# Optimization experiments

Hardware: AMD Instinct MI355X
Metric: run time of the kernel (lower is better)

Reference implementation:

```python
import jax, jax.numpy as jnp
import numpy as np

HIDDEN = 1024
NUM_HEADS = 16
HEAD_DIM = HIDDEN // NUM_HEADS


def setup_inputs() -> dict:
    key = jax.random.key(0)
    k1, k2, k3 = jax.random.split(key, 3)
    x = jax.random.normal(k1, (2, 2048, HIDDEN), dtype=jnp.float32)
    # Linear weights, torch layout [out_features, in_features]
    w_qkv = jax.random.normal(k2, (3 * HIDDEN, HIDDEN), dtype=jnp.float32) * 0.02
    w_out = jax.random.normal(k3, (HIDDEN, HIDDEN), dtype=jnp.float32) * 0.02
    return {"x": x, "w_qkv": w_qkv, "w_out": w_out}


def reference(x, w_qkv, w_out):
    B, S, H = x.shape
    scale = 1.0 / HEAD_DIM ** 0.5
    qkv = jnp.einsum('bsh,oh->bso', x, w_qkv)              # [B,S,3H]
    qkv = qkv.reshape(B, S, 3, NUM_HEADS, HEAD_DIM)
    qkv = jnp.transpose(qkv, (2, 0, 3, 1, 4))               # [3,B,nh,S,hd]
    q, k, v = qkv[0], qkv[1], qkv[2]
    scores = jnp.einsum('bnsd,bntd->bnst', q, k) * scale    # [B,nh,S,S]
    attn = jax.nn.softmax(scores, axis=-1)
    out = jnp.einsum('bnst,bntd->bnsd', attn, v)            # [B,nh,S,hd]
    out = jnp.transpose(out, (0, 2, 1, 3)).reshape(B, S, H)
    return jnp.einsum('bsh,oh->bso', out, w_out)
```

## Files before the change

### kernel.cpp

```cpp
#include <hip/hip_runtime.h>
#include <stdint.h>

typedef unsigned short u16;
typedef __bf16 bf16x8 __attribute__((ext_vector_type(8)));
typedef float f32x4 __attribute__((ext_vector_type(4)));
typedef float f32x16 __attribute__((ext_vector_type(16)));
typedef unsigned u32x4 __attribute__((ext_vector_type(4)));

#define DEVI __device__ __forceinline__

typedef __attribute__((address_space(1))) void gvoid;
typedef __attribute__((address_space(3))) void lvoid;

DEVI u16 f2b(float f) {
  unsigned x = __builtin_bit_cast(unsigned, f);
  return (u16)((x + 0x7fffu + ((x >> 16) & 1u)) >> 16);
}

DEVI float exp2g(float x) { return __builtin_amdgcn_exp2f(x); }

DEVI void gload_lds16(const void* g, void* l) {
  __builtin_amdgcn_global_load_lds((gvoid*)g, (lvoid*)l, 16, 0, 0);
}

#define QSCALE 0.18033688011112042f

__global__ void cast_all(const float* __restrict__ x, const float* __restrict__ wqkv,
                         const float* __restrict__ wout, u16* __restrict__ outb) {
  int i = blockIdx.x * 256 + threadIdx.x;
  int stride = gridDim.x * 256;
  for (; i < 2097152; i += stride) {
    const float* src;
    float sc = 1.0f;
    if (i < 1048576) {
      src = x + 4 * (long)i;
    } else if (i < 1835008) {
      int j = i - 1048576;
      src = wqkv + 4 * (long)j;
      if (j < 262144) sc = QSCALE;
    } else {
      src = wout + 4 * (long)(i - 1835008);
    }
    float4 v = *(const float4*)src;
    ushort4 o;
    o.x = f2b(v.x * sc); o.y = f2b(v.y * sc); o.z = f2b(v.z * sc); o.w = f2b(v.w * sc);
    ((ushort4*)outb)[i] = o;
  }
}

template<int OUT, int TM>
__global__ __launch_bounds__(256)
void gemm_bt(const u16* __restrict__ A, const u16* __restrict__ B, void* __restrict__ Cv,
             void* __restrict__ Cv2, int M, int N, int K) {
  constexpr int MI = TM / 32;
  __shared__ u16 lA[TM * 64];
  __shared__ u16 lB[128 * 64];
  const int tid = threadIdx.x;
  const int lane = tid & 63;
  const int lr = lane & 15;
  const int lg = lane >> 4;
  const int wid = tid >> 6;
  const long bm = (long)blockIdx.y * TM;
  const long bn = (long)blockIdx.x * 128;
  const int wr = (wid >> 1) * (TM / 2);
  const int wc = (wid & 1) * 64;

  f32x4 acc[MI][4];
#pragma unroll
  for (int i = 0; i < MI; ++i)
#pragma unroll
    for (int j = 0; j < 4; ++j)
      acc[i][j] = (f32x4){0.f, 0.f, 0.f, 0.f};

  for (int k0 = 0; k0 < K; k0 += 64) {
#pragma unroll
    for (int q = 0; q < MI; ++q) {
      int bi = tid + q * 256;
      int row = bi >> 3;
      int col = ((bi & 7) ^ (row & 7)) * 8;
      gload_lds16(A + (bm + row) * (long)K + k0 + col, (char*)lA + bi * 16);
    }
#pragma unroll
    for (int q = 0; q < 4; ++q) {
      int bi = tid + q * 256;
      int row = bi >> 3;
      int col = ((bi & 7) ^ (row & 7)) * 8;
      gload_lds16(B + (bn + row) * (long)K + k0 + col, (char*)lB + bi * 16);
    }
    __syncthreads();
#pragma unroll
    for (int kk = 0; kk < 2; ++kk) {
      bf16x8 af[MI], bfr[4];
      int kb = kk * 4 + lg;
#pragma unroll
      for (int mi = 0; mi < MI; ++mi) {
        int row = wr + mi * 16 + lr;
        af[mi] = *(const bf16x8*)((const char*)lA + row * 128 + ((kb ^ (row & 7)) << 4));
      }
#pragma unroll
      for (int ni = 0; ni < 4; ++ni) {
        int row = wc + ni * 16 + lr;
        bfr[ni] = *(const bf16x8*)((const char*)lB + row * 128 + ((kb ^ (row & 7)) << 4));
      }
#pragma unroll
      for (int mi = 0; mi < MI; ++mi)
#pragma unroll
        for (int ni = 0; ni < 4; ++ni)
          acc[mi][ni] = __builtin_amdgcn_mfma_f32_16x16x32_bf16(af[mi], bfr[ni], acc[mi][ni], 0, 0, 0);
    }
    __syncthreads();
  }

  if (OUT == 2 && bn >= 2048) {
#pragma unroll
    for (int mi = 0; mi < MI; ++mi)
#pragma unroll
      for (int ni = 0; ni < 4; ++ni) {
        long tok = bm + wr + mi * 16 + lg * 4;
        long f = bn + wc + ni * 16 + lr - 2048;
        ushort4 st;
        st.x = f2b(acc[mi][ni][0]);
        st.y = f2b(acc[mi][ni][1]);
        st.z = f2b(acc[mi][ni][2]);
        st.w = f2b(acc[mi][ni][3]);
        u16* dst = (u16*)Cv2 + (((tok >> 11) << 4) + (f >> 6)) * 131072 + (f & 63) * 2048 + (tok & 2047);
        *(ushort4*)dst = st;
      }
  } else {
    const long strideN = (OUT == 2) ? 2048 : N;
#pragma unroll
    for (int mi = 0; mi < MI; ++mi)
#pragma unroll
      for (int ni = 0; ni < 4; ++ni)
#pragma unroll
        for (int r = 0; r < 4; ++r) {
          long row = bm + wr + mi * 16 + lg * 4 + r;
          long col = bn + wc + ni * 16 + lr;
          float v = acc[mi][ni][r];
          if (OUT == 1) ((float*)Cv)[row * strideN + col] = v;
          else          ((u16*)Cv)[row * strideN + col] = f2b(v);
        }
  }
}

__global__ __launch_bounds__(256, 2)
void attn_fwd(const u16* __restrict__ qk, const u16* __restrict__ vT,
              u16* __restrict__ outb) {
  __shared__ char SM[33280];

  const int tid = threadIdx.x;
  const int lane = tid & 63;
  const int wid = tid >> 6;
  const int ql = lane & 31;
  const int h  = lane >> 5;
  const int th = wid >> 1;
  const int qw = wid & 1;

  const int flat = blockIdx.x + (blockIdx.y << 4) + (blockIdx.z << 8);
  const int swz  = ((flat & 7) << 6) + (flat >> 3);
  const int qt = swz & 15;
  const int hd = (swz >> 4) & 15;
  const int b  = swz >> 8;

  const long rowbase = (long)b * 2048;
  const int qcol = hd * 64;
  const int kcol = 1024 + hd * 64;
  const int TSK = 64 * 2048;
  const long vhb = ((long)b * 16 + hd) * 131072;

  const int q0w = qt * 128 + qw * 64;
  bf16x8 qfA[4], qfB[4];
  {
    const u16* qpA = qk + (rowbase + q0w + ql) * 2048 + qcol + h * 8;
    const u16* qpB = qpA + 32 * 2048;
#pragma unroll
    for (int dblk = 0; dblk < 4; ++dblk) {
      qfA[dblk] = *(const bf16x8*)(qpA + dblk * 16);
      qfB[dblk] = *(const bf16x8*)(qpB + dblk * 16);
    }
  }

  float lA = 0.f, lB = 0.f;
  f32x16 oA[2], oB[2];
#pragma unroll
  for (int d = 0; d < 2; ++d)
#pragma unroll
    for (int r = 0; r < 16; ++r) { oA[d][r] = 0.f; oB[d][r] = 0.f; }

  const int c0 = tid, c1 = tid + 256;
  const int rk0 = c0 >> 3, ck0 = ((c0 & 7) ^ (rk0 & 7)) * 8;
  const int rk1 = c1 >> 3, ck1 = ((c1 & 7) ^ (rk1 & 7)) * 8;
  const int d0 = c0 * 16, d1 = c1 * 16;
  const u16* kp0 = qk + (rowbase + rk0) * 2048 + kcol + ck0;
  const u16* kp1 = qk + (rowbase + rk1) * 2048 + kcol + ck1;
  const u16* vp0 = vT + vhb + rk0 * 2048 + ck0;
  const u16* vp1 = vT + vhb + rk1 * 2048 + ck1;

  gload_lds16(kp0, SM + d0);          gload_lds16(kp1, SM + d1);
  gload_lds16(vp0, SM + 16384 + d0);  gload_lds16(vp1, SM + 16384 + d1);
  kp0 += TSK; kp1 += TSK; vp0 += 64; vp1 += 64;
  asm volatile("s_waitcnt vmcnt(0)" ::: "memory");
  __builtin_amdgcn_s_barrier();
  __builtin_amdgcn_sched_barrier(0);

  for (int tt = 0; tt < 16; ++tt) {
#pragma unroll
    for (int P = 0; P < 2; ++P) {
      char* KsCur = SM + P * 8192;
      char* VsCur = SM + 16384 + P * 8192;
      char* KsNxt = SM + (P ^ 1) * 8192;
      char* VsNxt = SM + 16384 + (P ^ 1) * 8192;

      gload_lds16(kp0, KsNxt + d0);  gload_lds16(kp1, KsNxt + d1);
      gload_lds16(vp0, VsNxt + d0);  gload_lds16(vp1, VsNxt + d1);
      kp0 += TSK; kp1 += TSK; vp0 += 64; vp1 += 64;

      f32x16 sA, sB;
#pragma unroll
      for (int r = 0; r < 16; ++r) { sA[r] = 0.f; sB[r] = 0.f; }
      const char* Kb = KsCur + (th * 32 + ql) * 128;
      __builtin_amdgcn_s_setprio(1);
#pragma unroll
      for (int kd = 0; kd < 4; ++kd) {
        bf16x8 kf = *(const bf16x8*)(Kb + (((kd * 2 + h) ^ (ql & 7)) << 4));
        sA = __builtin_amdgcn_mfma_f32_32x32x16_bf16(kf, qfA[kd], sA, 0, 0, 0);
        sB = __builtin_amdgcn_mfma_f32_32x32x16_bf16(kf, qfB[kd], sB, 0, 0, 0);
      }
      __builtin_amdgcn_s_setprio(0);

#pragma unroll
      for (int r = 0; r < 16; ++r) sA[r] = exp2g(sA[r]);
#pragma unroll
      for (int r = 0; r < 16; ++r) sB[r] = exp2g(sB[r]);
      lA += (((sA[0] + sA[1]) + (sA[2] + sA[3])) + ((sA[4] + sA[5]) + (sA[6] + sA[7])))
          + (((sA[8] + sA[9]) + (sA[10] + sA[11])) + ((sA[12] + sA[13]) + (sA[14] + sA[15])));
      lB += (((sB[0] + sB[1]) + (sB[2] + sB[3])) + ((sB[4] + sB[5]) + (sB[6] + sB[7])))
          + (((sB[8] + sB[9]) + (sB[10] + sB[11])) + ((sB[12] + sB[13]) + (sB[14] + sB[15])));

      unsigned wA[8], wB[8];
#pragma unroll
      for (int m = 0; m < 8; ++m) {
        asm("v_cvt_pk_bf16_f32 %0, %1, %2" : "=v"(wA[m]) : "v"(sA[2 * m]), "v"(sA[2 * m + 1]));
        asm("v_cvt_pk_bf16_f32 %0, %1, %2" : "=v"(wB[m]) : "v"(sB[2 * m]), "v"(sB[2 * m + 1]));
      }

      bf16x8 pbA[2], pbB[2];
#pragma unroll
      for (int ks = 0; ks < 2; ++ks) {
        unsigned a0 = wA[4 * ks],     a2 = wA[4 * ks + 2];
        unsigned a1 = wA[4 * ks + 1], a3 = wA[4 * ks + 3];
        asm("s_nop 1\n\tv_permlane32_swap_b32 %0, %1" : "+v"(a0), "+v"(a2));
        asm("s_nop 1\n\tv_permlane32_swap_b32 %0, %1" : "+v"(a1), "+v"(a3));
        u32x4 t; t[0] = a0; t[1] = a1; t[2] = a2; t[3] = a3;
        pbA[ks] = __builtin_bit_cast(bf16x8, t);
        unsigned b0 = wB[4 * ks],     b2 = wB[4 * ks + 2];
        unsigned b1 = wB[4 * ks + 1], b3 = wB[4 * ks + 3];
        asm("s_nop 1\n\tv_permlane32_swap_b32 %0, %1" : "+v"(b0), "+v"(b2));
        asm("s_nop 1\n\tv_permlane32_swap_b32 %0, %1" : "+v"(b1), "+v"(b3));
        u32x4 u; u[0] = b0; u[1] = b1; u[2] = b2; u[3] = b3;
        pbB[ks] = __builtin_bit_cast(bf16x8, u);
      }

      __builtin_amdgcn_s_setprio(1);
#pragma unroll
      for (int dblk = 0; dblk < 2; ++dblk) {
        const char* Vb = VsCur + (dblk * 32 + ql) * 128;
#pragma unroll
        for (int ks = 0; ks < 2; ++ks) {
          bf16x8 vf = *(const bf16x8*)(Vb + (((th * 4 + ks * 2 + h) ^ (ql & 7)) << 4));
          oA[dblk] = __builtin_amdgcn_mfma_f32_32x32x16_bf16(vf, pbA[ks], oA[dblk], 0, 0, 0);
          oB[dblk] = __builtin_amdgcn_mfma_f32_32x32x16_bf16(vf, pbB[ks], oB[dblk], 0, 0, 0);
        }
      }
      __builtin_amdgcn_s_setprio(0);

      asm volatile("s_waitcnt vmcnt(0)" ::: "memory");
      __builtin_amdgcn_s_barrier();
      __builtin_amdgcn_sched_barrier(0);
    }
  }
  __syncthreads();

  float pxA = lA, pyA = lA;
  asm("s_nop 1\n\tv_permlane32_swap_b32 %0, %1" : "+v"(pxA), "+v"(pyA));
  float lwA = lA + (h ? pxA : pyA);
  float pxB = lB, pyB = lB;
  asm("s_nop 1\n\tv_permlane32_swap_b32 %0, %1" : "+v"(pxB), "+v"(pyB));
  float lwB = lB + (h ? pxB : pyB);

  if (th == 1) {
    char* regA = SM + (qw * 2 + 0) * 8192;
    char* regB = SM + (qw * 2 + 1) * 8192;
#pragma unroll
    for (int dblk = 0; dblk < 2; ++dblk)
#pragma unroll
      for (int r = 0; r < 16; ++r) {
        int dl = dblk * 32 + (r & 3) + 8 * (r >> 2) + 4 * h;
        *(float*)(regA + dl * 128 + ql * 4) = oA[dblk][r];
        *(float*)(regB + dl * 128 + ql * 4) = oB[dblk][r];
      }
    if (h == 0) {
      *(float*)(SM + 32768 + (qw * 2 + 0) * 128 + ql * 4) = lwA;
      *(float*)(SM + 32768 + (qw * 2 + 1) * 128 + ql * 4) = lwB;
    }
  }
  __syncthreads();
  if (th == 0) {
    const char* regA = SM + (qw * 2 + 0) * 8192;
    const char* regB = SM + (qw * 2 + 1) * 8192;
#pragma unroll
    for (int dblk = 0; dblk < 2; ++dblk)
#pragma unroll
      for (int r = 0; r < 16; ++r) {
        int dl = dblk * 32 + (r & 3) + 8 * (r >> 2) + 4 * h;
        oA[dblk][r] += *(const float*)(regA + dl * 128 + ql * 4);
        oB[dblk][r] += *(const float*)(regB + dl * 128 + ql * 4);
      }
    float invA = 1.0f / (lwA + *(const float*)(SM + 32768 + (qw * 2 + 0) * 128 + ql * 4));
    float invB = 1.0f / (lwB + *(const float*)(SM + 32768 + (qw * 2 + 1) * 128 + ql * 4));
    long rowA = rowbase + q0w + ql;
    long rowB = rowA + 32;
#pragma unroll
    for (int dblk = 0; dblk < 2; ++dblk)
#pragma unroll
      for (int m = 0; m < 4; ++m) {
        ushort4 stA;
        stA.x = f2b(oA[dblk][4 * m + 0] * invA);
        stA.y = f2b(oA[dblk][4 * m + 1] * invA);
        stA.z = f2b(oA[dblk][4 * m + 2] * invA);
        stA.w = f2b(oA[dblk][4 * m + 3] * invA);
        *(ushort4*)(outb + rowA * 1024 + qcol + dblk * 32 + 8 * m + 4 * h) = stA;
        ushort4 stB;
        stB.x = f2b(oB[dblk][4 * m + 0] * invB);
        stB.y = f2b(oB[dblk][4 * m + 1] * invB);
        stB.z = f2b(oB[dblk][4 * m + 2] * invB);
        stB.w = f2b(oB[dblk][4 * m + 3] * invB);
        *(ushort4*)(outb + rowB * 1024 + qcol + dblk * 32 + 8 * m + 4 * h) = stB;
      }
  }
}

extern "C" void kernel_launch(void* const* d_in, const int* in_sizes, int n_in,
                              void* d_out, int out_size, void* d_ws, size_t ws_size,
                              hipStream_t stream) {
  const float* x     = (const float*)d_in[0];
  const float* w_qkv = (const float*)d_in[1];
  const float* w_out = (const float*)d_in[2];
  float* out = (float*)d_out;

  char* ws = (char*)d_ws;
  u16* xb    = (u16*)(ws);
  u16* wqkvb = (u16*)(ws + 8388608);
  u16* woutb = (u16*)(ws + 14680064);
  u16* qk    = (u16*)(ws + 16777216);
  u16* vT    = (u16*)(ws + 33554432);
  u16* attn  = (u16*)(ws + 41943040);

  cast_all<<<2048, 256, 0, stream>>>(x, w_qkv, w_out, xb);

  gemm_bt<2, 128><<<dim3(24, 32), 256, 0, stream>>>(xb, wqkvb, qk, vT, 4096, 3072, 1024);

  attn_fwd<<<dim3(16, 16, 2), 256, 0, stream>>>(qk, vT, attn);

  gemm_bt<1, 64><<<dim3(8, 64), 256, 0, stream>>>(attn, woutb, out, nullptr, 4096, 1024, 1024);
}
```

Before: 103.0 us.

## Double-buffer GEMM LDS tiles, remap blocks across XCDs, raise MFMA priority

The GEMM kernel now double-buffers its LDS tiles, so the global-to-LDS loads for the next K step are issued before the MFMAs on the current tile and memory latency overlaps compute. It also remaps block indices so consecutive tiles spread across the eight XCD chiplets, aiming for better L2 locality, and raises wave priority around the MFMA section. In exchange LDS use doubles, which may cut occupancy, and the remap assumes the block count divides evenly by eight.

```diff
diff --git a/kernel.cpp b/kernel.cpp
--- a/kernel.cpp
+++ b/kernel.cpp
@@ -53,15 +53,23 @@
 void gemm_bt(const u16* __restrict__ A, const u16* __restrict__ B, void* __restrict__ Cv,
              void* __restrict__ Cv2, int M, int N, int K) {
   constexpr int MI = TM / 32;
-  __shared__ u16 lA[TM * 64];
-  __shared__ u16 lB[128 * 64];
+  constexpr int ASZ = TM * 64;
+  __shared__ u16 lA[2 * ASZ];
+  __shared__ u16 lB[2 * 128 * 64];
   const int tid = threadIdx.x;
   const int lane = tid & 63;
   const int lr = lane & 15;
   const int lg = lane >> 4;
   const int wid = tid >> 6;
-  const long bm = (long)blockIdx.y * TM;
-  const long bn = (long)blockIdx.x * 128;
+
+  const int f = blockIdx.x + gridDim.x * blockIdx.y;
+  const int chunk = (gridDim.x * gridDim.y) >> 3;
+  const int ln = (f & 7) * chunk + (f >> 3);
+  const int bx = ln / gridDim.y;
+  const int by = ln % gridDim.y;
+  const long bm = (long)by * TM;
+  const long bn = (long)bx * 128;
+
   const int wr = (wid >> 1) * (TM / 2);
   const int wc = (wid & 1) * 64;
 
@@ -72,22 +80,37 @@
     for (int j = 0; j < 4; ++j)
       acc[i][j] = (f32x4){0.f, 0.f, 0.f, 0.f};
 
-  for (int k0 = 0; k0 < K; k0 += 64) {
+  auto stageA = [&](int buf, int k0) {
 #pragma unroll
     for (int q = 0; q < MI; ++q) {
       int bi = tid + q * 256;
       int row = bi >> 3;
       int col = ((bi & 7) ^ (row & 7)) * 8;
-      gload_lds16(A + (bm + row) * (long)K + k0 + col, (char*)lA + bi * 16);
-    }
+      gload_lds16(A + (bm + row) * (long)K + k0 + col, (char*)(lA + buf * ASZ) + bi * 16);
+    }
+  };
+  auto stageB = [&](int buf, int k0) {
 #pragma unroll
     for (int q = 0; q < 4; ++q) {
       int bi = tid + q * 256;
       int row = bi >> 3;
       int col = ((bi & 7) ^ (row & 7)) * 8;
-      gload_lds16(B + (bn + row) * (long)K + k0 + col, (char*)lB + bi * 16);
-    }
-    __syncthreads();
+      gload_lds16(B + (bn + row) * (long)K + k0 + col, (char*)(lB + buf * 128 * 64) + bi * 16);
+    }
+  };
+
+  stageA(0, 0); stageB(0, 0);
+  asm volatile("s_waitcnt vmcnt(0)" ::: "memory");
+  __builtin_amdgcn_s_barrier();
+  __builtin_amdgcn_sched_barrier(0);
+
+  const int NITER = K >> 6;
+  for (int it = 0; it < NITER; ++it) {
+    const int cur = it & 1;
+    if (it + 1 < NITER) { stageA(cur ^ 1, (it + 1) * 64); stageB(cur ^ 1, (it + 1) * 64); }
+
+    const u16* cA = lA + cur * ASZ;
+    const u16* cB = lB + cur * 128 * 64;
 #pragma unroll
     for (int kk = 0; kk < 2; ++kk) {
       bf16x8 af[MI], bfr[4];
@@ -95,20 +118,27 @@
 #pragma unroll
       for (int mi = 0; mi < MI; ++mi) {
         int row = wr + mi * 16 + lr;
-        af[mi] = *(const bf16x8*)((const char*)lA + row * 128 + ((kb ^ (row & 7)) << 4));
+        af[mi] = *(const bf16x8*)((const char*)cA + row * 128 + ((kb ^ (row & 7)) << 4));
       }
 #pragma unroll
       for (int ni = 0; ni < 4; ++ni) {
         int row = wc + ni * 16 + lr;
-        bfr[ni] = *(const bf16x8*)((const char*)lB + row * 128 + ((kb ^ (row & 7)) << 4));
-      }
+        bfr[ni] = *(const bf16x8*)((const char*)cB + row * 128 + ((kb ^ (row & 7)) << 4));
+      }
+      __builtin_amdgcn_s_setprio(1);
 #pragma unroll
       for (int mi = 0; mi < MI; ++mi)
 #pragma unroll
         for (int ni = 0; ni < 4; ++ni)
           acc[mi][ni] = __builtin_amdgcn_mfma_f32_16x16x32_bf16(af[mi], bfr[ni], acc[mi][ni], 0, 0, 0);
-    }
-    __syncthreads();
+      __builtin_amdgcn_s_setprio(0);
+    }
+
+    if (it + 1 < NITER) {
+      asm volatile("s_waitcnt vmcnt(0)" ::: "memory");
+      __builtin_amdgcn_s_barrier();
+      __builtin_amdgcn_sched_barrier(0);
+    }
   }
 
   if (OUT == 2 && bn >= 2048) {
@@ -117,13 +147,13 @@
 #pragma unroll
       for (int ni = 0; ni < 4; ++ni) {
         long tok = bm + wr + mi * 16 + lg * 4;
-        long f = bn + wc + ni * 16 + lr - 2048;
+        long ff = bn + wc + ni * 16 + lr - 2048;
         ushort4 st;
         st.x = f2b(acc[mi][ni][0]);
         st.y = f2b(acc[mi][ni][1]);
         st.z = f2b(acc[mi][ni][2]);
         st.w = f2b(acc[mi][ni][3]);
-        u16* dst = (u16*)Cv2 + (((tok >> 11) << 4) + (f >> 6)) * 131072 + (f & 63) * 2048 + (tok & 2047);
+        u16* dst = (u16*)Cv2 + (((tok >> 11) << 4) + (ff >> 6)) * 131072 + (ff & 63) * 2048 + (tok & 2047);
         *(ushort4*)dst = st;
       }
   } else {
```

After: 114.3 us. 10.9% more time.

## Split attention over two KV halves and add a combine kernel

Applied to the files above, without the earlier changes.

The attention kernel now splits the key/value sequence into two halves, so the grid doubles to 1024 blocks. Each block writes unnormalized bf16 partial outputs plus per-row softmax denominators to workspace buffers. A new elementwise kernel sums the two partials and normalizes them before the output projection GEMM. The aim is better CU occupancy during attention, at the cost of an extra launch, extra global traffic for the partials, and bf16 rounding of the unnormalized partials. The combine step does no max rescaling, so it is only correct if both halves use the same softmax offset.

```diff
diff --git a/kernel.cpp b/kernel.cpp
--- a/kernel.cpp
+++ b/kernel.cpp
@@ -16,6 +16,8 @@
   unsigned x = __builtin_bit_cast(unsigned, f);
   return (u16)((x + 0x7fffu + ((x >> 16) & 1u)) >> 16);
 }
+
+DEVI float b2f(u16 u) { return __builtin_bit_cast(float, (unsigned)u << 16); }
 
 DEVI float exp2g(float x) { return __builtin_amdgcn_exp2f(x); }
 
@@ -117,13 +119,13 @@
 #pragma unroll
       for (int ni = 0; ni < 4; ++ni) {
         long tok = bm + wr + mi * 16 + lg * 4;
-        long f = bn + wc + ni * 16 + lr - 2048;
+        long ff = bn + wc + ni * 16 + lr - 2048;
         ushort4 st;
         st.x = f2b(acc[mi][ni][0]);
         st.y = f2b(acc[mi][ni][1]);
         st.z = f2b(acc[mi][ni][2]);
         st.w = f2b(acc[mi][ni][3]);
-        u16* dst = (u16*)Cv2 + (((tok >> 11) << 4) + (f >> 6)) * 131072 + (f & 63) * 2048 + (tok & 2047);
+        u16* dst = (u16*)Cv2 + (((tok >> 11) << 4) + (ff >> 6)) * 131072 + (ff & 63) * 2048 + (tok & 2047);
         *(ushort4*)dst = st;
       }
   } else {
@@ -145,7 +147,7 @@
 
 __global__ __launch_bounds__(256, 2)
 void attn_fwd(const u16* __restrict__ qk, const u16* __restrict__ vT,
-              u16* __restrict__ outb) {
+              u16* __restrict__ po0, u16* __restrict__ po1, float* __restrict__ pl) {
   __shared__ char SM[33280];
 
   const int tid = threadIdx.x;
@@ -157,10 +159,12 @@
   const int qw = wid & 1;
 
   const int flat = blockIdx.x + (blockIdx.y << 4) + (blockIdx.z << 8);
-  const int swz  = ((flat & 7) << 6) + (flat >> 3);
+  const int swz  = ((flat & 7) << 7) + (flat >> 3);
   const int qt = swz & 15;
   const int hd = (swz >> 4) & 15;
-  const int b  = swz >> 8;
+  const int zz = swz >> 8;
+  const int b  = zz >> 1;
+  const int ts = zz & 1;
 
   const long rowbase = (long)b * 2048;
   const int qcol = hd * 64;
@@ -191,10 +195,10 @@
   const int rk0 = c0 >> 3, ck0 = ((c0 & 7) ^ (rk0 & 7)) * 8;
   const int rk1 = c1 >> 3, ck1 = ((c1 & 7) ^ (rk1 & 7)) * 8;
   const int d0 = c0 * 16, d1 = c1 * 16;
-  const u16* kp0 = qk + (rowbase + rk0) * 2048 + kcol + ck0;
-  const u16* kp1 = qk + (rowbase + rk1) * 2048 + kcol + ck1;
-  const u16* vp0 = vT + vhb + rk0 * 2048 + ck0;
-  const u16* vp1 = vT + vhb + rk1 * 2048 + ck1;
+  const u16* kp0 = qk + (rowbase + ts * 1024 + rk0) * 2048 + kcol + ck0;
+  const u16* kp1 = qk + (rowbase + ts * 1024 + rk1) * 2048 + kcol + ck1;
+  const u16* vp0 = vT + vhb + rk0 * 2048 + ts * 1024 + ck0;
+  const u16* vp1 = vT + vhb + rk1 * 2048 + ts * 1024 + ck1;
 
   gload_lds16(kp0, SM + d0);          gload_lds16(kp1, SM + d1);
   gload_lds16(vp0, SM + 16384 + d0);  gload_lds16(vp1, SM + 16384 + d1);
@@ -203,7 +207,7 @@
   __builtin_amdgcn_s_barrier();
   __builtin_amdgcn_sched_barrier(0);
 
-  for (int tt = 0; tt < 16; ++tt) {
+  for (int tt = 0; tt < 8; ++tt) {
 #pragma unroll
     for (int P = 0; P < 2; ++P) {
       char* KsCur = SM + P * 8192;
@@ -316,28 +320,64 @@
         oA[dblk][r] += *(const float*)(regA + dl * 128 + ql * 4);
         oB[dblk][r] += *(const float*)(regB + dl * 128 + ql * 4);
       }
-    float invA = 1.0f / (lwA + *(const float*)(SM + 32768 + (qw * 2 + 0) * 128 + ql * 4));
-    float invB = 1.0f / (lwB + *(const float*)(SM + 32768 + (qw * 2 + 1) * 128 + ql * 4));
+    float ltotA = lwA + *(const float*)(SM + 32768 + (qw * 2 + 0) * 128 + ql * 4);
+    float ltotB = lwB + *(const float*)(SM + 32768 + (qw * 2 + 1) * 128 + ql * 4);
+    if (h == 0) {
+      float* plb = pl + (long)ts * 65536 + ((long)b * 16 + hd) * 2048;
+      plb[q0w + ql]      = ltotA;
+      plb[q0w + 32 + ql] = ltotB;
+    }
     long rowA = rowbase + q0w + ql;
     long rowB = rowA + 32;
+    u16* pob = ts ? po1 : po0;
 #pragma unroll
     for (int dblk = 0; dblk < 2; ++dblk)
 #pragma unroll
       for (int m = 0; m < 4; ++m) {
         ushort4 stA;
-        stA.x = f2b(oA[dblk][4 * m + 0] * invA);
-        stA.y = f2b(oA[dblk][4 * m + 1] * invA);
-        stA.z = f2b(oA[dblk][4 * m + 2] * invA);
-        stA.w = f2b(oA[dblk][4 * m + 3] * invA);
-        *(ushort4*)(outb + rowA * 1024 + qcol + dblk * 32 + 8 * m + 4 * h) = stA;
+        stA.x = f2b(oA[dblk][4 * m + 0]);
+        stA.y = f2b(oA[dblk][4 * m + 1]);
+        stA.z = f2b(oA[dblk][4 * m + 2]);
+        stA.w = f2b(oA[dblk][4 * m + 3]);
+        *(ushort4*)(pob + rowA * 1024 + qcol + dblk * 32 + 8 * m + 4 * h) = stA;
         ushort4 stB;
-        stB.x = f2b(oB[dblk][4 * m + 0] * invB);
-        stB.y = f2b(oB[dblk][4 * m + 1] * invB);
-        stB.z = f2b(oB[dblk][4 * m + 2] * invB);
-        stB.w = f2b(oB[dblk][4 * m + 3] * invB);
-        *(ushort4*)(outb + rowB * 1024 + qcol + dblk * 32 + 8 * m + 4 * h) = stB;
-      }
-  }
+        stB.x = f2b(oB[dblk][4 * m + 0]);
+        stB.y = f2b(oB[dblk][4 * m + 1]);
+        stB.z = f2b(oB[dblk][4 * m + 2]);
+        stB.w = f2b(oB[dblk][4 * m + 3]);
+        *(ushort4*)(pob + rowB * 1024 + qcol + dblk * 32 + 8 * m + 4 * h) = stB;
+      }
+  }
+}
+
+__global__ __launch_bounds__(256)
+void attn_combine(u16* __restrict__ po0, const u16* __restrict__ po1,
+                  const float* __restrict__ pl) {
+  long i = (long)blockIdx.x * 256 + threadIdx.x;
+  long base = i * 8;
+  int row = (int)(base >> 10);
+  int col = (int)(base & 1023);
+  int hd = col >> 6;
+  int b = row >> 11;
+  int q = row & 2047;
+  long lidx = ((long)b * 16 + hd) * 2048 + q;
+  float inv = 1.0f / (pl[lidx] + pl[65536 + lidx]);
+
+  ushort4 a0 = *(const ushort4*)(po0 + base);
+  ushort4 a1 = *(const ushort4*)(po0 + base + 4);
+  ushort4 b0 = *(const ushort4*)(po1 + base);
+  ushort4 b1 = *(const ushort4*)(po1 + base + 4);
+  ushort4 o0, o1;
+  o0.x = f2b((b2f(a0.x) + b2f(b0.x)) * inv);
+  o0.y = f2b((b2f(a0.y) + b2f(b0.y)) * inv);
+  o0.z = f2b((b2f(a0.z) + b2f(b0.z)) * inv);
+  o0.w = f2b((b2f(a0.w) + b2f(b0.w)) * inv);
+  o1.x = f2b((b2f(a1.x) + b2f(b1.x)) * inv);
+  o1.y = f2b((b2f(a1.y) + b2f(b1.y)) * inv);
+  o1.z = f2b((b2f(a1.z) + b2f(b1.z)) * inv);
+  o1.w = f2b((b2f(a1.w) + b2f(b1.w)) * inv);
+  *(ushort4*)(po0 + base) = o0;
+  *(ushort4*)(po0 + base + 4) = o1;
 }
 
 extern "C" void kernel_launch(void* const* d_in, const int* in_sizes, int n_in,
@@ -354,13 +394,17 @@
   u16* woutb = (u16*)(ws + 14680064);
   u16* qk    = (u16*)(ws + 16777216);
   u16* vT    = (u16*)(ws + 33554432);
-  u16* attn  = (u16*)(ws + 41943040);
+  u16* po0   = (u16*)(ws + 41943040);
+  u16* po1   = (u16*)(ws);
+  float* pl  = (float*)(ws + 8388608);
 
   cast_all<<<2048, 256, 0, stream>>>(x, w_qkv, w_out, xb);
 
   gemm_bt<2, 128><<<dim3(24, 32), 256, 0, stream>>>(xb, wqkvb, qk, vT, 4096, 3072, 1024);
 
-  attn_fwd<<<dim3(16, 16, 2), 256, 0, stream>>>(qk, vT, attn);
-
-  gemm_bt<1, 64><<<dim3(8, 64), 256, 0, stream>>>(attn, woutb, out, nullptr, 4096, 1024, 1024);
-}
+  attn_fwd<<<dim3(16, 16, 4), 256, 0, stream>>>(qk, vT, po0, po1, pl);
+
+  attn_combine<<<2048, 256, 0, stream>>>(po0, po1, pl);
+
+  gemm_bt<1, 64><<<dim3(8, 64), 256, 0, stream>>>(po0, woutb, out, nullptr, 4096, 1024, 1024);
+}
```

After: 111.6 us. 1.08x slower.
